# Optimization experiments

Hardware: AMD Instinct MI355X
Metric: run time of the kernel (lower is better)

The kernel has to match this reference:

```python
import jax, jax.numpy as jnp
import numpy as np

D = 1024      # d_model
H = 16        # n_heads
M = 64        # n_memories
DK = D // H   # head dim
EPS = 1e-5    # LayerNorm eps


def setup_inputs() -> dict:
    key = jax.random.key(0)
    ks = jax.random.split(key, 16)
    B, N = 4, 1024
    s = 0.02
    return {
        "queries": jax.random.normal(ks[0], (B, N, D), jnp.float32),
        "keys": jax.random.normal(ks[1], (B, N, D), jnp.float32),
        "values": jax.random.normal(ks[2], (B, N, D), jnp.float32),
        "attention_mask": jax.random.randint(ks[3], (B, 1, 1, N), 0, 2, dtype=jnp.int32),
        "Wq": jax.random.normal(ks[4], (D, D), jnp.float32) * s,
        "bq": jnp.zeros((D,), jnp.float32),
        "Wk": jax.random.normal(ks[5], (D, D), jnp.float32) * s,
        "bk": jnp.zeros((D,), jnp.float32),
        "Wv": jax.random.normal(ks[6], (D, D), jnp.float32) * s,
        "bv": jnp.zeros((D,), jnp.float32),
        "Wo": jax.random.normal(ks[7], (D, D), jnp.float32) * s,
        "bo": jnp.zeros((D,), jnp.float32),
        "m_k": jax.random.normal(ks[8], (1, M, D), jnp.float32) * 0.01,
        "m_v": jax.random.normal(ks[9], (1, M, D), jnp.float32) * 0.01,
        "gamma": jnp.ones((D,), jnp.float32),
        "beta": jnp.zeros((D,), jnp.float32),
    }


def _layer_norm(x, gamma, beta):
    mu = jnp.mean(x, axis=-1, keepdims=True)
    var = jnp.var(x, axis=-1, keepdims=True)
    return (x - mu) * jax.lax.rsqrt(var + EPS) * gamma + beta


def reference(queries, keys, values, attention_mask,
              Wq, bq, Wk, bk, Wv, bv, Wo, bo, m_k, m_v, gamma, beta):
    B, Nq, _ = queries.shape
    Nk = keys.shape[1]
    scale = 1.0 / np.sqrt(DK)

    # projections (torch Linear: x @ W.T + b)
    q = (queries @ Wq.T + bq).reshape(B, Nq, H, DK).transpose(0, 2, 1, 3)  # b h nq d

    # memory-augmented K/V (memory tokens scaled as in the source)
    k_full = jnp.concatenate(
        [keys @ Wk.T + bk, jnp.broadcast_to(m_k * np.sqrt(DK), (B, M, D))], axis=1)
    v_full = jnp.concatenate(
        [values @ Wv.T + bv, jnp.broadcast_to(m_v * np.sqrt(M), (B, M, D))], axis=1)
    k = k_full.reshape(B, Nk + M, H, DK).transpose(0, 2, 1, 3)  # b h nk+m d
    v = v_full.reshape(B, Nk + M, H, DK).transpose(0, 2, 1, 3)  # b h nk+m d

    scores = jnp.einsum('bhqd,bhkd->bhqk', q, k) * scale  # [B,H,Nq,Nk+M]

    # partial masking: only the first Nk (non-memory) columns are maskable
    mask = jnp.concatenate(
        [attention_mask.astype(bool),
         jnp.zeros((B, 1, 1, M), dtype=bool)], axis=-1)
    scores = jnp.where(mask, -jnp.inf, scores)

    p_attn = jax.nn.softmax(scores, axis=-1)  # dropout p=0.0 -> identity
    out = jnp.einsum('bhqk,bhkd->bhqd', p_attn, v)
    out = out.transpose(0, 2, 1, 3).reshape(B, Nq, D)
    out = out @ Wo.T + bo

    # residual + LayerNorm (outer dropout is identity at p=0.0)
    return _layer_norm(queries + out, gamma, beta)
```

## Files before the change

kernel.cpp:

```cpp
#include <hip/hip_runtime.h>


typedef __bf16 bf16;
typedef __bf16 bf16x8 __attribute__((ext_vector_type(8)));
typedef __bf16 bf16x4 __attribute__((ext_vector_type(4)));
typedef __bf16 bf16x2 __attribute__((ext_vector_type(2)));
typedef float  f32x4  __attribute__((ext_vector_type(4)));
typedef float  f32x16 __attribute__((ext_vector_type(16)));
typedef unsigned uintx4 __attribute__((ext_vector_type(4)));

#define NSEQ 1024
#define NKV  1088
#define DMODEL 1024

struct CvtArgs { const float* s[7]; const float* mk; const float* mv; };

__global__ __launch_bounds__(256) void prep(CvtArgs c, bf16* __restrict__ dst,
                                            bf16* __restrict__ Kb,
                                            bf16* __restrict__ Vt)
{
    int blk = blockIdx.x;
    if (blk < 8192) {
        size_t e = ((size_t)blk * 256 + threadIdx.x) * 8;
        const float* s;
        if (e < ((size_t)3 << 22)) {
            s = c.s[e >> 22] + (e & 0x3FFFFF);
        } else {
            size_t wq = e - ((size_t)3 << 22);
            s = c.s[3 + (wq >> 20)] + (wq & 0xFFFFF);
        }
        f32x4 a = *(const f32x4*)s;
        f32x4 b = *(const f32x4*)(s + 4);
        bf16x8 o;
        for (int i = 0; i < 4; i++) { o[i] = (bf16)a[i]; o[4 + i] = (bf16)b[i]; }
        *(bf16x8*)&dst[e] = o;
    } else {
        int i = (blk - 8192) * 256 + threadIdx.x;
        int b = i >> 16, md = i & 65535;
        int m = md >> 10, dcol = md & 1023;
        Kb[(size_t)b * (NKV * DMODEL) + (size_t)(NSEQ + m) * DMODEL + dcol]
            = (bf16)(c.mk[md] * 8.0f);
        Vt[((size_t)b * 1024 + dcol) * NKV + NSEQ + m] = (bf16)(c.mv[md] * 8.0f);
    }
}

typedef __attribute__((address_space(1))) void gas_void;
typedef __attribute__((address_space(3))) void las_void;

__device__ __forceinline__ void gload16(const bf16* g, bf16* l)
{
    __builtin_amdgcn_global_load_lds((gas_void*)g, (las_void*)l, 16, 0, 0);
}

struct GemmArgsB {
    const bf16* A;
    const bf16* W;
    const float* bias;
    bf16* C;
    int osK;
    int vt;
};

__global__ __launch_bounds__(256, 3) void gemm128_lds(GemmArgsB g0, GemmArgsB g1,
                                                      GemmArgsB g2)
{
    const GemmArgsB g = (blockIdx.z == 0) ? g0 : (blockIdx.z == 1) ? g1 : g2;
    __shared__ bf16 As[128][32];
    __shared__ bf16 Bs[128][32];
    const int t = threadIdx.x;
    const int lane = t & 63, w = t >> 6;
    const int qi = lane & 15, qq = lane >> 4;
    const int wrow = (w >> 1) * 64, wcol = (w & 1) * 64;
    const int bm = blockIdx.y * 128, bn = blockIdx.x * 128;

    const int srow = w * 32 + (lane >> 2);
    const int scol = (lane & 3) * 8;
    const bf16* Ag = g.A + (size_t)(bm + srow) * DMODEL + scol;
    const bf16* Wg = g.W + (size_t)(bn + srow) * DMODEL + scol;
    bf16* Al = &As[w * 32][0];
    bf16* Bl = &Bs[w * 32][0];

    f32x4 acc[4][4] = {};

#define STAGE(kt)                                                             \
    do {                                                                      \
        gload16(Ag + (kt),                 Al);                               \
        gload16(Ag + (kt) + 16 * DMODEL,   Al + 16 * 32);                     \
        gload16(Wg + (kt),                 Bl);                               \
        gload16(Wg + (kt) + 16 * DMODEL,   Bl + 16 * 32);                    \
    } while (0)

    STAGE(0);
    for (int kt = 0; kt < DMODEL; kt += 32) {
        __syncthreads();
        bf16x8 a[4], b[4];
        for (int i = 0; i < 4; i++)
            a[i] = *(const bf16x8*)&As[wrow + i * 16 + qi][qq * 8];
        for (int j = 0; j < 4; j++)
            b[j] = *(const bf16x8*)&Bs[wcol + j * 16 + qi][qq * 8];
        __syncthreads();
        if (kt + 32 < DMODEL) STAGE(kt + 32);
        for (int i = 0; i < 4; i++)
            for (int j = 0; j < 4; j++)
                acc[i][j] = __builtin_amdgcn_mfma_f32_16x16x32_bf16(
                    a[i], b[j], acc[i][j], 0, 0, 0);
    }
#undef STAGE

    for (int i = 0; i < 4; i++)
        for (int j = 0; j < 4; j++) {
            int row0 = bm + wrow + i * 16 + qq * 4;
            int col  = bn + wcol + j * 16 + qi;
            float bcol = g.bias[col];
            if (g.vt) {
                bf16x4 v;
                for (int r = 0; r < 4; r++) v[r] = (bf16)(acc[i][j][r] + bcol);
                size_t off = ((size_t)((row0 >> 10) * 16 + (col >> 6)) * 64 + (col & 63))
                           * NKV + (row0 & 1023);
                *(bf16x4*)&g.C[off] = v;
            } else {
                for (int r = 0; r < 4; r++) {
                    int row = row0 + r;
                    size_t off = (size_t)(row >> 10) * g.osK
                               + (size_t)(row & 1023) * DMODEL + col;
                    g.C[off] = (bf16)(acc[i][j][r] + bcol);
                }
            }
        }
}

struct GemmArgs {
    const void* A;
    const float* W;
    const float* bias;
    bf16* C;
    int osK;
    int vt;
};

template<bool ABF>
__global__ __launch_bounds__(256, 2) void gemm128(GemmArgs g0, GemmArgs g1, GemmArgs g2)
{
    const GemmArgs g = (blockIdx.z == 0) ? g0 : (blockIdx.z == 1) ? g1 : g2;
    __shared__ bf16 As[128][44];
    __shared__ bf16 Bs[128][44];
    const int t = threadIdx.x;
    const int lane = t & 63, w = t >> 6;
    const int qi = lane & 15, qq = lane >> 4;
    const int wrow = (w >> 1) * 64, wcol = (w & 1) * 64;
    const int bm = blockIdx.y * 128, bn = blockIdx.x * 128;
    const int sr = t >> 1, sc = (t & 1) * 16;

    f32x4 acc[4][4] = {};

    f32x4 pa[4];
    bf16x8 pab[2];
    f32x4 pw[4];

    const float* Wp = g.W + (size_t)(bn + sr) * DMODEL + sc;
    const float* Af = (const float*)g.A + (size_t)(bm + sr) * DMODEL + sc;
    const bf16*  Ab = (const bf16*)g.A + (size_t)(bm + sr) * DMODEL + sc;

#define LOAD_TILES(kt)                                                        \
    do {                                                                      \
        if (ABF) {                                                            \
            pab[0] = *(const bf16x8*)(Ab + (kt));                             \
            pab[1] = *(const bf16x8*)(Ab + (kt) + 8);                         \
        } else {                                                              \
            pa[0] = *(const f32x4*)(Af + (kt));                               \
            pa[1] = *(const f32x4*)(Af + (kt) + 4);                           \
            pa[2] = *(const f32x4*)(Af + (kt) + 8);                           \
            pa[3] = *(const f32x4*)(Af + (kt) + 12);                          \
        }                                                                     \
        pw[0] = *(const f32x4*)(Wp + (kt));                                   \
        pw[1] = *(const f32x4*)(Wp + (kt) + 4);                               \
        pw[2] = *(const f32x4*)(Wp + (kt) + 8);                               \
        pw[3] = *(const f32x4*)(Wp + (kt) + 12);                              \
    } while (0)

#define STORE_TILES()                                                         \
    do {                                                                      \
        if (ABF) {                                                            \
            *(bf16x8*)&As[sr][sc]     = pab[0];                               \
            *(bf16x8*)&As[sr][sc + 8] = pab[1];                               \
        } else {                                                              \
            bf16x8 v0, v1;                                                    \
            for (int i = 0; i < 4; i++) {                                     \
                v0[i] = (bf16)pa[0][i]; v0[4 + i] = (bf16)pa[1][i];           \
                v1[i] = (bf16)pa[2][i]; v1[4 + i] = (bf16)pa[3][i];           \
            }                                                                 \
            *(bf16x8*)&As[sr][sc]     = v0;                                   \
            *(bf16x8*)&As[sr][sc + 8] = v1;                                   \
        }                                                                     \
        {                                                                     \
            bf16x8 u0, u1;                                                    \
            for (int i = 0; i < 4; i++) {                                     \
                u0[i] = (bf16)pw[0][i]; u0[4 + i] = (bf16)pw[1][i];           \
                u1[i] = (bf16)pw[2][i]; u1[4 + i] = (bf16)pw[3][i];           \
            }                                                                 \
            *(bf16x8*)&Bs[sr][sc]     = u0;                                   \
            *(bf16x8*)&Bs[sr][sc + 8] = u1;                                   \
        }                                                                     \
    } while (0)

    LOAD_TILES(0);
    STORE_TILES();
    __syncthreads();

    for (int kt = 0; kt < DMODEL; kt += 32) {
        const bool more = (kt + 32) < DMODEL;
        if (more) LOAD_TILES(kt + 32);
        bf16x8 a[4], b[4];
        for (int i = 0; i < 4; i++)
            a[i] = *(const bf16x8*)&As[wrow + i * 16 + qi][qq * 8];
        for (int j = 0; j < 4; j++)
            b[j] = *(const bf16x8*)&Bs[wcol + j * 16 + qi][qq * 8];
        for (int i = 0; i < 4; i++)
            for (int j = 0; j < 4; j++)
                acc[i][j] = __builtin_amdgcn_mfma_f32_16x16x32_bf16(a[i], b[j], acc[i][j], 0, 0, 0);
        if (more) {
            __syncthreads();
            STORE_TILES();
            __syncthreads();
        }
    }
#undef LOAD_TILES
#undef STORE_TILES

    for (int i = 0; i < 4; i++)
        for (int j = 0; j < 4; j++) {
            int row0 = bm + wrow + i * 16 + qq * 4;
            int col  = bn + wcol + j * 16 + qi;
            float bcol = g.bias[col];
            if (g.vt) {
                bf16x4 v;
                for (int r = 0; r < 4; r++) v[r] = (bf16)(acc[i][j][r] + bcol);
                size_t off = ((size_t)((row0 >> 10) * 16 + (col >> 6)) * 64 + (col & 63))
                           * NKV + (row0 & 1023);
                *(bf16x4*)&g.C[off] = v;
            } else {
                for (int r = 0; r < 4; r++) {
                    int row = row0 + r;
                    size_t off = (size_t)(row >> 10) * g.osK
                               + (size_t)(row & 1023) * DMODEL + col;
                    g.C[off] = (bf16)(acc[i][j][r] + bcol);
                }
            }
        }
}

__global__ void fill_mem(const float* __restrict__ mk, const float* __restrict__ mv,
                         bf16* __restrict__ K, bf16* __restrict__ Vt)
{
    int i = blockIdx.x * 256 + threadIdx.x;
    int b = i >> 16, md = i & 65535;
    int m = md >> 10, dcol = md & 1023;
    K[(size_t)b * (NKV * DMODEL) + (size_t)(NSEQ + m) * DMODEL + dcol]
        = (bf16)(mk[md] * 8.0f);
    Vt[((size_t)b * 1024 + dcol) * NKV + NSEQ + m] = (bf16)(mv[md] * 8.0f);
}

__device__ __forceinline__ unsigned pkbf(float a, float b)
{
    bf16x2 t; t[0] = (bf16)a; t[1] = (bf16)b;
    unsigned u; __builtin_memcpy(&u, &t, 4); return u;
}

__global__ __launch_bounds__(256) void attn_flash(const bf16* Q,
        const bf16* __restrict__ K, const bf16* __restrict__ Vt,
        const int* __restrict__ mask, bf16* O)
{
    __shared__ bf16 sKV[2][64][72];
    __shared__ __align__(16) float sM[NKV];
    const int t = threadIdx.x, lane = t & 63, w = t >> 6;
    int bh, q0;
    if (gridDim.y == 64) {
        int lin = blockIdx.y * gridDim.x + blockIdx.x;
        bh = ((lin & 7) << 3) | ((lin >> 3) & 7);
        q0 = (lin >> 6) * 128;
    } else {
        bh = blockIdx.y;
        q0 = blockIdx.x * 128;
    }
    const int b = bh >> 4, h = bh & 15;
    const int sr = t >> 2, sc = (t & 3) * 16;
    const int lq = lane & 31, hi = lane >> 5;

    for (int j = t; j < NKV; j += 256)
        sM[j] = (j < NSEQ && mask[b * NSEQ + j] != 0) ? -3.0e38f : 0.0f;

    const size_t qrow = (size_t)(b * NSEQ + q0 + w * 32 + lq) * DMODEL + h * 64;
    bf16x8 qf[4];
#pragma unroll
    for (int c = 0; c < 4; c++) {
        bf16x8 v = *(const bf16x8*)&Q[qrow + c * 16 + hi * 8];
        for (int i = 0; i < 8; i++) v[i] = (bf16)((float)v[i] * 0.125f);
        qf[c] = v;
    }

    const bf16* kbase = K + (size_t)(b * NKV + sr) * DMODEL + h * 64 + sc;
    const bf16* vbase = Vt + ((size_t)bh * 64 + sr) * NKV + sc;

    bf16x8 pk0, pk1, pv0, pv1;
#define LOAD_KV(jt)                                                           \
    do {                                                                      \
        const bf16* kp = kbase + (size_t)(jt) * 64 * DMODEL;                  \
        pk0 = *(const bf16x8*)kp;                                             \
        pk1 = *(const bf16x8*)(kp + 8);                                       \
        const bf16* vp = vbase + (jt) * 64;                                   \
        pv0 = *(const bf16x8*)vp;                                             \
        pv1 = *(const bf16x8*)(vp + 8);                                       \
    } while (0)
#define STORE_KV()                                                            \
    do {                                                                      \
        *(bf16x8*)&sKV[0][sr][sc]     = pk0;                                  \
        *(bf16x8*)&sKV[0][sr][sc + 8] = pk1;                                  \
        *(bf16x8*)&sKV[1][sr][sc]     = pv0;                                  \
        *(bf16x8*)&sKV[1][sr][sc + 8] = pv1;                                  \
    } while (0)

    LOAD_KV(0);
    STORE_KV();

    float m_i = -3.0e38f, l_i = 0.f;
    f32x16 oacc0 = {}, oacc1 = {};

    for (int jt = 0; jt < 17; jt++) {
        const int j0 = jt * 64;
        __syncthreads();
        const bool more = jt < 16;
        if (more) LOAD_KV(jt + 1);

        f32x16 accs[2];
#pragma unroll
        for (int kb = 0; kb < 2; kb++) {
#pragma unroll
            for (int g2 = 0; g2 < 4; g2++) {
                f32x4 m4 = *(const f32x4*)&sM[j0 + kb * 32 + 8 * g2 + 4 * hi];
                accs[kb][4 * g2 + 0] = m4[0];
                accs[kb][4 * g2 + 1] = m4[1];
                accs[kb][4 * g2 + 2] = m4[2];
                accs[kb][4 * g2 + 3] = m4[3];
            }
#pragma unroll
            for (int c = 0; c < 4; c++) {
                bf16x8 kf = *(const bf16x8*)&sKV[0][kb * 32 + lq][c * 16 + hi * 8];
                accs[kb] = __builtin_amdgcn_mfma_f32_32x32x16_bf16(
                    kf, qf[c], accs[kb], 0, 0, 0);
            }
        }

        float rm = accs[0][0];
#pragma unroll
        for (int r = 1; r < 16; r++) rm = fmaxf(rm, accs[0][r]);
#pragma unroll
        for (int r = 0; r < 16; r++) rm = fmaxf(rm, accs[1][r]);
        rm = fmaxf(rm, __shfl_xor(rm, 32, 64));
        float mnew = fmaxf(m_i, rm);
        float alpha = __expf(m_i - mnew);
        m_i = mnew;
        float rs = 0.f;
#pragma unroll
        for (int kb = 0; kb < 2; kb++)
#pragma unroll
            for (int r = 0; r < 16; r++) {
                float p = __expf(accs[kb][r] - mnew);
                accs[kb][r] = p;
                rs += p;
            }
        rs += __shfl_xor(rs, 32, 64);
        l_i = l_i * alpha + rs;

        unsigned dwv[16];
#pragma unroll
        for (int kb = 0; kb < 2; kb++)
#pragma unroll
            for (int a = 0; a < 4; a++) {
                dwv[kb * 8 + 2 * a]     = pkbf(accs[kb][4 * a], accs[kb][4 * a + 1]);
                dwv[kb * 8 + 2 * a + 1] = pkbf(accs[kb][4 * a + 2], accs[kb][4 * a + 3]);
            }
        bf16x8 pb[4];
#pragma unroll
        for (int i = 0; i < 4; i++) {
            const int kb = i >> 1, ae = 2 * (i & 1), ao = ae + 1;
            unsigned se0 = dwv[kb * 8 + 2 * ae], se1 = dwv[kb * 8 + 2 * ae + 1];
            unsigned so0 = dwv[kb * 8 + 2 * ao], so1 = dwv[kb * 8 + 2 * ao + 1];
            unsigned s0 = hi ? se0 : so0, s1 = hi ? se1 : so1;
            unsigned k0 = hi ? so0 : se0, k1 = hi ? so1 : se1;
            unsigned r0 = __shfl_xor((int)s0, 32, 64);
            unsigned r1 = __shfl_xor((int)s1, 32, 64);
            uintx4 cw;
            cw[0] = hi ? r0 : k0; cw[1] = hi ? r1 : k1;
            cw[2] = hi ? k0 : r0; cw[3] = hi ? k1 : r1;
            __builtin_memcpy(&pb[i], &cw, 16);
        }

#pragma unroll
        for (int r = 0; r < 16; r++) { oacc0[r] *= alpha; oacc1[r] *= alpha; }
#pragma unroll
        for (int c = 0; c < 4; c++) {
            bf16x8 vf0 = *(const bf16x8*)&sKV[1][lq][c * 16 + hi * 8];
            bf16x8 vf1 = *(const bf16x8*)&sKV[1][32 + lq][c * 16 + hi * 8];
            oacc0 = __builtin_amdgcn_mfma_f32_32x32x16_bf16(vf0, pb[c], oacc0, 0, 0, 0);
            oacc1 = __builtin_amdgcn_mfma_f32_32x32x16_bf16(vf1, pb[c], oacc1, 0, 0, 0);
        }
        __syncthreads();
        if (more) STORE_KV();
    }
#undef LOAD_KV
#undef STORE_KV

    float linv = 1.0f / l_i;
    __syncthreads();
    bf16 (*sO)[72] = reinterpret_cast<bf16(*)[72]>(&sKV[0][0][0]);
#pragma unroll
    for (int r = 0; r < 16; r++) {
        int dl = (r & 3) + 8 * (r >> 2) + 4 * hi;
        sO[w * 32 + lq][dl]      = (bf16)(oacc0[r] * linv);
        sO[w * 32 + lq][32 + dl] = (bf16)(oacc1[r] * linv);
    }
    __syncthreads();
    {
        int row = t >> 1, ch = (t & 1) * 32;
        bf16* dst = &O[(size_t)(b * NSEQ + q0 + row) * DMODEL + h * 64 + ch];
#pragma unroll
        for (int k = 0; k < 4; k++)
            *(bf16x8*)(dst + k * 8) = *(const bf16x8*)&sO[row][ch + k * 8];
    }
}

__global__ __launch_bounds__(256) void residual_ln(const float* __restrict__ X,
        const bf16* __restrict__ Y, const float* __restrict__ gamma,
        const float* __restrict__ beta, float* __restrict__ out)
{
    __shared__ float red[8];
    int row = blockIdx.x, t = threadIdx.x;
    size_t base = (size_t)row * DMODEL + t * 4;
    f32x4  xv = *(const f32x4*)&X[base];
    bf16x4 yv = *(const bf16x4*)&Y[base];
    float s[4], sum = 0.f, sq = 0.f;
    for (int i = 0; i < 4; i++) {
        s[i] = xv[i] + (float)yv[i];
        sum += s[i]; sq += s[i] * s[i];
    }
    for (int o = 32; o; o >>= 1) { sum += __shfl_xor(sum, o, 64); sq += __shfl_xor(sq, o, 64); }
    if ((t & 63) == 0) { red[t >> 6] = sum; red[4 + (t >> 6)] = sq; }
    __syncthreads();
    sum = red[0] + red[1] + red[2] + red[3];
    sq  = red[4] + red[5] + red[6] + red[7];
    float mean = sum * (1.0f / DMODEL);
    float var  = sq  * (1.0f / DMODEL) - mean * mean;
    float rstd = rsqrtf(var + 1e-5f);
    f32x4 gv = *(const f32x4*)&gamma[t * 4];
    f32x4 bv = *(const f32x4*)&beta[t * 4];
    f32x4 ov;
    for (int i = 0; i < 4; i++)
        ov[i] = (s[i] - mean) * rstd * gv[i] + bv[i];
    *(f32x4*)&out[base] = ov;
}

extern "C" void kernel_launch(void* const* d_in, const int* in_sizes, int n_in,
                              void* d_out, int out_size, void* d_ws, size_t ws_size,
                              hipStream_t stream)
{
    const float* queries = (const float*)d_in[0];
    const float* keys    = (const float*)d_in[1];
    const float* values  = (const float*)d_in[2];
    const int*   amask   = (const int*)d_in[3];
    const float* Wq = (const float*)d_in[4];  const float* bq = (const float*)d_in[5];
    const float* Wk = (const float*)d_in[6];  const float* bk = (const float*)d_in[7];
    const float* Wv = (const float*)d_in[8];  const float* bv = (const float*)d_in[9];
    const float* Wo = (const float*)d_in[10]; const float* bo = (const float*)d_in[11];
    const float* mk = (const float*)d_in[12]; const float* mv = (const float*)d_in[13];
    const float* gamma = (const float*)d_in[14]; const float* beta = (const float*)d_in[15];
    float* out = (float*)d_out;

    bf16* Qb = (bf16*)(out + (size_t)2 * 1024 * 1024);
    const size_t SB  = (size_t)NSEQ * DMODEL;
    const size_t KVB = (size_t)NKV * DMODEL;
    dim3 gb(256);

    const size_t need_r10 = (2 * 4 * KVB + 3 * 4 * SB + 4 * SB) * sizeof(bf16);

    if (ws_size >= need_r10) {
        bf16* Kb = (bf16*)d_ws;
        bf16* Vt = Kb + 4 * KVB;
        bf16* Ab = Vt + 4 * KVB;
        bf16* Wb = Ab + 12 * SB;
        bf16* PR = Ab;

        CvtArgs ca;
        ca.s[0] = queries; ca.s[1] = keys; ca.s[2] = values;
        ca.s[3] = Wq; ca.s[4] = Wk; ca.s[5] = Wv; ca.s[6] = Wo;
        ca.mk = mk; ca.mv = mv;
        prep<<<dim3(8192 + 1024), gb, 0, stream>>>(ca, Ab, Kb, Vt);

        GemmArgsB gq{Ab,           Wb,           bq, Qb, (int)SB,  0};
        GemmArgsB gk{Ab + 4 * SB,  Wb + SB,      bk, Kb, (int)KVB, 0};
        GemmArgsB gv{Ab + 8 * SB,  Wb + 2 * SB,  bv, Vt, 0,        1};
        gemm128_lds<<<dim3(8, 32, 3), gb, 0, stream>>>(gq, gk, gv);
        attn_flash<<<dim3(8, 64), gb, 0, stream>>>(Qb, Kb, Vt, amask, Qb);
        GemmArgsB go{Qb, Wb + 3 * SB, bo, PR, (int)SB, 0};
        gemm128_lds<<<dim3(8, 32, 1), gb, 0, stream>>>(go, go, go);
        residual_ln<<<dim3(4096), gb, 0, stream>>>(queries, PR, gamma, beta, out);
    } else if (ws_size >= (size_t)2 * 4 * KVB * sizeof(bf16)) {
        bf16* Kb = (bf16*)d_ws;
        bf16* Vt = Kb + 4 * KVB;
        bf16* PR = Kb;

        GemmArgs gq{queries, Wq, bq, Qb, (int)SB,  0};
        GemmArgs gk{keys,    Wk, bk, Kb, (int)KVB, 0};
        GemmArgs gv{values,  Wv, bv, Vt, 0,        1};
        gemm128<false><<<dim3(8, 32, 3), gb, 0, stream>>>(gq, gk, gv);
        fill_mem<<<dim3(1024), gb, 0, stream>>>(mk, mv, Kb, Vt);
        attn_flash<<<dim3(8, 64), gb, 0, stream>>>(Qb, Kb, Vt, amask, Qb);
        GemmArgs go{Qb, Wo, bo, PR, (int)SB, 0};
        gemm128<true><<<dim3(8, 32, 1), gb, 0, stream>>>(go, go, go);
        residual_ln<<<dim3(4096), gb, 0, stream>>>(queries, PR, gamma, beta, out);
    } else {
        bf16* Kb = (bf16*)d_ws;
        bf16* Vt = Kb + KVB;
        bf16* PR = Kb;

        GemmArgs gq{queries, Wq, bq, Qb, (int)SB, 0};
        gemm128<false><<<dim3(8, 32, 1), gb, 0, stream>>>(gq, gq, gq);
        for (int b = 0; b < 4; b++) {
            GemmArgs gk{keys   + b * SB, Wk, bk, Kb, 0, 0};
            GemmArgs gv{values + b * SB, Wv, bv, Vt, 0, 1};
            gemm128<false><<<dim3(8, 8, 2), gb, 0, stream>>>(gk, gv, gv);
            fill_mem<<<dim3(256), gb, 0, stream>>>(mk, mv, Kb, Vt);
            attn_flash<<<dim3(8, 16), gb, 0, stream>>>(Qb + b * SB, Kb, Vt,
                                                       amask + b * NSEQ, Qb + b * SB);
            GemmArgs go{Qb + b * SB, Wo, bo, PR, 0, 0};
            gemm128<true><<<dim3(8, 8, 1), gb, 0, stream>>>(go, go, go);
            residual_ln<<<dim3(1024), gb, 0, stream>>>(queries + b * SB, PR,
                                                       gamma, beta, out + b * SB);
        }
    }
}
```

Baseline: 236.4 us.

## Double-buffer K/V tiles, add lazy softmax rescaling, and use permlane32 swap

The flash attention kernel now keeps two LDS buffers for K/V tiles, so each iteration needs one barrier instead of two and the next tile's stores overlap compute on the current one. The online softmax only rescales the running max and accumulators when some lane's new row max exceeds the old one by more than 8, which skips most alpha multiplies. When the permlane32_swap builtin is available it replaces the shfl_xor plus select shuffle used to rebuild P fragments. The max and sum reductions are split into two independent chains. The extra buffer doubles K/V LDS use, and the lazy rescale lets unnormalized exponentials reach up to e^8, a small numerical risk.

After: 229.6 us. 1.03x faster.

```diff
diff --git a/kernel.cpp b/kernel.cpp
--- a/kernel.cpp
+++ b/kernel.cpp
@@ -270,7 +270,7 @@
         const bf16* __restrict__ K, const bf16* __restrict__ Vt,
         const int* __restrict__ mask, bf16* O)
 {
-    __shared__ bf16 sKV[2][64][72];
+    __shared__ bf16 sKV[2][2][64][72];
     __shared__ __align__(16) float sM[NKV];
     const int t = threadIdx.x, lane = t & 63, w = t >> 6;
     int bh, q0;
@@ -311,25 +311,26 @@
         pv0 = *(const bf16x8*)vp;                                             \
         pv1 = *(const bf16x8*)(vp + 8);                                       \
     } while (0)
-#define STORE_KV()                                                            \
+#define STORE_KV(bi)                                                          \
     do {                                                                      \
-        *(bf16x8*)&sKV[0][sr][sc]     = pk0;                                  \
-        *(bf16x8*)&sKV[0][sr][sc + 8] = pk1;                                  \
-        *(bf16x8*)&sKV[1][sr][sc]     = pv0;                                  \
-        *(bf16x8*)&sKV[1][sr][sc + 8] = pv1;                                  \
+        *(bf16x8*)&sKV[bi][0][sr][sc]     = pk0;                              \
+        *(bf16x8*)&sKV[bi][0][sr][sc + 8] = pk1;                              \
+        *(bf16x8*)&sKV[bi][1][sr][sc]     = pv0;                              \
+        *(bf16x8*)&sKV[bi][1][sr][sc + 8] = pv1;                              \
     } while (0)
 
     LOAD_KV(0);
-    STORE_KV();
-
-    float m_i = -3.0e38f, l_i = 0.f;
+    STORE_KV(0);
+
+    float m_i = -1.0e30f, l_i = 0.f;
     f32x16 oacc0 = {}, oacc1 = {};
 
     for (int jt = 0; jt < 17; jt++) {
         const int j0 = jt * 64;
-        __syncthreads();
+        const int cb = jt & 1;
         const bool more = jt < 16;
         if (more) LOAD_KV(jt + 1);
+        __syncthreads();
 
         f32x16 accs[2];
 #pragma unroll
@@ -344,32 +345,39 @@
             }
 #pragma unroll
             for (int c = 0; c < 4; c++) {
-                bf16x8 kf = *(const bf16x8*)&sKV[0][kb * 32 + lq][c * 16 + hi * 8];
+                bf16x8 kf = *(const bf16x8*)&sKV[cb][0][kb * 32 + lq][c * 16 + hi * 8];
                 accs[kb] = __builtin_amdgcn_mfma_f32_32x32x16_bf16(
                     kf, qf[c], accs[kb], 0, 0, 0);
             }
         }
 
-        float rm = accs[0][0];
-#pragma unroll
-        for (int r = 1; r < 16; r++) rm = fmaxf(rm, accs[0][r]);
-#pragma unroll
-        for (int r = 0; r < 16; r++) rm = fmaxf(rm, accs[1][r]);
+        float rm0 = accs[0][0], rm1 = accs[1][0];
+#pragma unroll
+        for (int r = 1; r < 16; r++) {
+            rm0 = fmaxf(rm0, accs[0][r]);
+            rm1 = fmaxf(rm1, accs[1][r]);
+        }
+        float rm = fmaxf(rm0, rm1);
         rm = fmaxf(rm, __shfl_xor(rm, 32, 64));
-        float mnew = fmaxf(m_i, rm);
-        float alpha = __expf(m_i - mnew);
-        m_i = mnew;
-        float rs = 0.f;
-#pragma unroll
-        for (int kb = 0; kb < 2; kb++)
-#pragma unroll
-            for (int r = 0; r < 16; r++) {
-                float p = __expf(accs[kb][r] - mnew);
-                accs[kb][r] = p;
-                rs += p;
-            }
+        if (!__all(rm - m_i <= 8.0f)) {
+            float mnew = fmaxf(m_i, rm);
+            float alpha = __expf(m_i - mnew);
+            m_i = mnew;
+            l_i *= alpha;
+#pragma unroll
+            for (int r = 0; r < 16; r++) { oacc0[r] *= alpha; oacc1[r] *= alpha; }
+        }
+        float rs0 = 0.f, rs1 = 0.f;
+#pragma unroll
+        for (int r = 0; r < 16; r++) {
+            float p0 = __expf(accs[0][r] - m_i);
+            float p1 = __expf(accs[1][r] - m_i);
+            accs[0][r] = p0; accs[1][r] = p1;
+            rs0 += p0; rs1 += p1;
+        }
+        float rs = rs0 + rs1;
         rs += __shfl_xor(rs, 32, 64);
-        l_i = l_i * alpha + rs;
+        l_i += rs;
 
         unsigned dwv[16];
 #pragma unroll
@@ -381,38 +389,41 @@
             }
         bf16x8 pb[4];
 #pragma unroll
-        for (int i = 0; i < 4; i++) {
-            const int kb = i >> 1, ae = 2 * (i & 1), ao = ae + 1;
-            unsigned se0 = dwv[kb * 8 + 2 * ae], se1 = dwv[kb * 8 + 2 * ae + 1];
-            unsigned so0 = dwv[kb * 8 + 2 * ao], so1 = dwv[kb * 8 + 2 * ao + 1];
-            unsigned s0 = hi ? se0 : so0, s1 = hi ? se1 : so1;
-            unsigned k0 = hi ? so0 : se0, k1 = hi ? so1 : se1;
-            unsigned r0 = __shfl_xor((int)s0, 32, 64);
-            unsigned r1 = __shfl_xor((int)s1, 32, 64);
+        for (int c = 0; c < 4; c++) {
+            const int base = (c >> 1) * 8 + (c & 1) * 4;
+            unsigned e0 = dwv[base],     e1 = dwv[base + 1];
+            unsigned o0 = dwv[base + 2], o1 = dwv[base + 3];
             uintx4 cw;
-            cw[0] = hi ? r0 : k0; cw[1] = hi ? r1 : k1;
-            cw[2] = hi ? k0 : r0; cw[3] = hi ? k1 : r1;
-            __builtin_memcpy(&pb[i], &cw, 16);
-        }
-
-#pragma unroll
-        for (int r = 0; r < 16; r++) { oacc0[r] *= alpha; oacc1[r] *= alpha; }
+#if __has_builtin(__builtin_amdgcn_permlane32_swap)
+            auto r0 = __builtin_amdgcn_permlane32_swap(e0, o0, false, false);
+            auto r1 = __builtin_amdgcn_permlane32_swap(e1, o1, false, false);
+            cw[0] = r0[0]; cw[1] = r1[0]; cw[2] = r0[1]; cw[3] = r1[1];
+#else
+            unsigned s0 = hi ? e0 : o0, s1 = hi ? e1 : o1;
+            unsigned k0 = hi ? o0 : e0, k1 = hi ? o1 : e1;
+            unsigned x0 = __shfl_xor((int)s0, 32, 64);
+            unsigned x1 = __shfl_xor((int)s1, 32, 64);
+            cw[0] = hi ? x0 : k0; cw[1] = hi ? x1 : k1;
+            cw[2] = hi ? k0 : x0; cw[3] = hi ? k1 : x1;
+#endif
+            __builtin_memcpy(&pb[c], &cw, 16);
+        }
+
 #pragma unroll
         for (int c = 0; c < 4; c++) {
-            bf16x8 vf0 = *(const bf16x8*)&sKV[1][lq][c * 16 + hi * 8];
-            bf16x8 vf1 = *(const bf16x8*)&sKV[1][32 + lq][c * 16 + hi * 8];
+            bf16x8 vf0 = *(const bf16x8*)&sKV[cb][1][lq][c * 16 + hi * 8];
+            bf16x8 vf1 = *(const bf16x8*)&sKV[cb][1][32 + lq][c * 16 + hi * 8];
             oacc0 = __builtin_amdgcn_mfma_f32_32x32x16_bf16(vf0, pb[c], oacc0, 0, 0, 0);
             oacc1 = __builtin_amdgcn_mfma_f32_32x32x16_bf16(vf1, pb[c], oacc1, 0, 0, 0);
         }
-        __syncthreads();
-        if (more) STORE_KV();
+        if (more) STORE_KV(cb ^ 1);
     }
 #undef LOAD_KV
 #undef STORE_KV
 
     float linv = 1.0f / l_i;
     __syncthreads();
-    bf16 (*sO)[72] = reinterpret_cast<bf16(*)[72]>(&sKV[0][0][0]);
+    bf16 (*sO)[72] = reinterpret_cast<bf16(*)[72]>(&sKV[0][0][0][0]);
 #pragma unroll
     for (int r = 0; r < 16; r++) {
         int dl = (r & 3) + 8 * (r >> 2) + 4 * hi;
```
